# Kernel tuning notes

Measured on AMD Instinct MI355X. Metric: run time of the kernel, lower is better.

The kernel has to match this reference:

```python
import jax, jax.numpy as jnp
import numpy as np

B, H, G, N, D, S, K = 1, 32, 128, 64, 128, 256, 8
BIT_PACK = 8


def setup_inputs() -> dict:
    key = jax.random.key(0)
    ks = jax.random.split(key, 6)
    data = jax.random.normal(ks[0], (B, H, G, N, D), dtype=jnp.float32)
    query = jax.random.normal(ks[1], (B, H, 1, D), dtype=jnp.float32)
    outlier_indices = jax.random.randint(ks[2], (B, H, G, K), 0, D, dtype=jnp.int32)
    norm_data = jax.random.uniform(ks[3], (B, H, G, N), dtype=jnp.float32)
    norm_outlier = jax.random.uniform(ks[4], (B, H, G, N), dtype=jnp.float32)
    # _init_proj_dir + _init_rot_dir (rot=True): per-chunk QR, scaled by sqrt(D)
    proj = np.asarray(jax.random.normal(ks[5], (D, S), dtype=jnp.float32), dtype=np.float64)
    num_chunks = (S + D - 1) // D
    qs = []
    for i in range(num_chunks):
        q, _ = np.linalg.qr(proj[:, i * D:(i + 1) * D])
        qs.append(q)
    proj_dir_score = jnp.asarray(np.concatenate(qs, axis=-1) * np.sqrt(D), dtype=jnp.float32)  # [D, S]
    proj_dir_quant = proj_dir_score.T  # [S, D]
    return {"data": data, "query": query, "outlier_indices": outlier_indices,
            "norm_data": norm_data, "norm_outlier": norm_outlier,
            "proj_dir_quant": proj_dir_quant, "proj_dir_score": proj_dir_score}


def _pack_bits(sketched):
    # sketched: [..., S] -> uint8 packed [..., S//8] ; bit = (sketched > 0)
    x = (sketched > 0).astype(jnp.int32).reshape(*sketched.shape[:-1], -1, BIT_PACK)
    enc = (2 ** jnp.arange(BIT_PACK, dtype=jnp.int32))
    return (x * enc).sum(axis=-1).astype(jnp.uint8)


def reference(data, query, outlier_indices, norm_data, norm_outlier, proj_dir_quant, proj_dir_score):
    s = proj_dir_quant.shape[0]
    d = data.shape[-1]
    # scatter outlier indices into a {0,1} mask over head_dim, per (B,H,G)
    mask = (jax.nn.one_hot(outlier_indices, d, dtype=jnp.float32).sum(axis=-2) > 0).astype(data.dtype)  # [B,H,G,D]
    key_outlier = data * mask[..., None, :]
    key_inlier = data * (1.0 - mask)[..., None, :]
    # JL random projection: [B,H,G,N,D] x [S,D] -> [B,H,G,N,S]
    sk_outlier = jnp.einsum('bhgnd,sd->bhgns', key_outlier, proj_dir_quant)
    sk_inlier = jnp.einsum('bhgnd,sd->bhgns', key_inlier, proj_dir_quant)
    # 1-bit sign quantization + byte packing
    hash_inlier = _pack_bits(sk_inlier)                  # [B,H,G,N,S//8]
    hash_outlier = _pack_bits(sk_outlier)[..., : s // 16]  # truncated outlier sketch
    # score path (PyTorch fallback math): inlier hamming-style inner product
    sketched_q = jnp.einsum('bhqd,ds->bhqs', query, proj_dir_score)[:, :, 0, :]  # [B,H,S]
    bits = jnp.where(sk_inlier > 0, 1.0, -1.0).astype(jnp.float32)  # == unpacked hash_inlier bits *2-1
    ip = jnp.einsum('bhs,bhgns->bhgn', sketched_q, bits)
    scl = jnp.sqrt(jnp.asarray(np.pi / 2, dtype=jnp.float32)) / s
    scores = (scl * norm_data * ip).reshape(data.shape[0], data.shape[1], -1, 1)  # [B,H,G*N,1]
    return hash_inlier, hash_outlier, scores
```

## Files before the change

kernel.cpp:

```cpp
#include <hip/hip_runtime.h>
#include <hip/hip_bf16.h>


typedef __attribute__((ext_vector_type(8))) short short8;
typedef __attribute__((ext_vector_type(4))) float f32x4;

constexpr int cH = 32, cG = 128, cN = 64, cD = 128, cS = 256, cK = 8;
constexpr int HASH_OUT_BASE = cH * cG * cN * (cS / 8);
constexpr int SCORE_BASE    = HASH_OUT_BASE + cH * cG * cN * (cS / 16);
constexpr float EPS_IN  = 1e-3f;
constexpr float EPS_OUT = 1e-3f;
constexpr size_t WS_BHI = 32768, WS_BLO = 98304, WS_NEED = 163840;

#define MFMA(a, b, c) __builtin_amdgcn_mfma_f32_16x16x32_bf16(a, b, c, 0, 0, 0)

__device__ inline short f2bf(float x) {
    unsigned u = __builtin_bit_cast(unsigned, x);
    u += 0x7FFFu + ((u >> 16) & 1u);
    return (short)(u >> 16);
}
__device__ inline float bf2f(short s) {
    return __builtin_bit_cast(float, (unsigned)((unsigned short)s) << 16);
}
__device__ inline unsigned long long sel4(unsigned long long a0, unsigned long long a1,
                                          unsigned long long a2, unsigned long long a3, int r) {
    unsigned long long x = a0;
    x = (r == 1) ? a1 : x; x = (r == 2) ? a2 : x; x = (r == 3) ? a3 : x;
    return x;
}
__device__ inline int sel8(const int* u, int k) {
    int x = u[0];
    x = (k == 1) ? u[1] : x; x = (k == 2) ? u[2] : x; x = (k == 3) ? u[3] : x;
    x = (k == 4) ? u[4] : x; x = (k == 5) ? u[5] : x; x = (k == 6) ? u[6] : x;
    x = (k == 7) ? u[7] : x;
    return x;
}
#define CE(i, j) { int a = u[i], b = u[j]; u[i] = min(a, b); u[j] = max(a, b); }

#define SORT8_AND_MASK(oidx_ptr, bb)                                   \
    int u[cK];                                                         \
    _Pragma("unroll")                                                  \
    for (int k = 0; k < cK; ++k) u[k] = (oidx_ptr)[(bb) * cK + k];     \
    unsigned long long m0 = 0, m1 = 0;                                 \
    _Pragma("unroll")                                                  \
    for (int k = 0; k < cK; ++k) {                                     \
        int v = u[k];                                                  \
        if (v < 64) m0 |= 1ull << v; else m1 |= 1ull << (v - 64);      \
    }                                                                  \
    CE(0,1) CE(2,3) CE(4,5) CE(6,7)                                    \
    CE(0,2) CE(1,3) CE(4,6) CE(5,7)                                    \
    CE(1,2) CE(5,6)                                                    \
    CE(0,4) CE(1,5) CE(2,6) CE(3,7)                                    \
    CE(2,4) CE(3,5)                                                    \
    CE(1,2) CE(3,4) CE(5,6)

__device__ __attribute__((noinline)) float exact_inlier(
    const float* __restrict__ dr, const float* __restrict__ pr,
    unsigned long long m0, unsigned long long m1)
{
    float ex = 0.0f;
    #pragma unroll 1
    for (int dc = 0; dc < 4; ++dc) {
        float4 da[8], pa[8];
        #pragma unroll
        for (int j = 0; j < 8; ++j) {
            da[j] = reinterpret_cast<const float4*>(dr)[dc * 8 + j];
            pa[j] = reinterpret_cast<const float4*>(pr)[dc * 8 + j];
        }
        #pragma unroll
        for (int j = 0; j < 8; ++j) {
            float dv[4] = { da[j].x, da[j].y, da[j].z, da[j].w };
            float pv[4] = { pa[j].x, pa[j].y, pa[j].z, pa[j].w };
            #pragma unroll
            for (int e = 0; e < 4; ++e) {
                const int d = dc * 32 + j * 4 + e;
                const bool msk = ((((d < 64) ? (m0 >> d) : (m1 >> (d - 64))) & 1ull) != 0);
                ex = fmaf(dv[e], msk ? 0.0f : pv[e], ex);
            }
        }
    }
    return ex;
}

__global__ __launch_bounds__(256) void qjl_qv(
    const float* __restrict__ query, const float* __restrict__ projs,
    float* __restrict__ qv_out)
{
    const int h = blockIdx.x, s = threadIdx.x;
    float qa = 0.0f;
    for (int d = 0; d < cD; ++d)
        qa = fmaf(query[h * cD + d], projs[d * cS + s], qa);
    qv_out[h * cS + s] = qa;
}

__global__ __launch_bounds__(256) void qjl_bfrag(
    const float* __restrict__ projq, short* __restrict__ bhi, short* __restrict__ blo)
{
    const int idx = blockIdx.x * 256 + threadIdx.x;
    const int l = idx & 63, nt = (idx >> 6) & 15, ksub = idx >> 10;
    const int s = nt * 16 + (l & 15);
    const int k0 = ksub * 32 + (l >> 4) * 8;
    #pragma unroll
    for (int j = 0; j < 8; ++j) {
        float x = projq[s * cD + k0 + j];
        short h = f2bf(x);
        bhi[idx * 8 + j] = h;
        blo[idx * 8 + j] = f2bf(x - bf2f(h));
    }
}

__global__ __launch_bounds__(256, 3) void qjl_mfma(
    const float* __restrict__ data, const int* __restrict__ oidx,
    const float* __restrict__ norm_data, const float* __restrict__ projq,
    const float* __restrict__ qv_ws, const short* __restrict__ bhi_ws,
    const short* __restrict__ blo_ws, float* __restrict__ out)
{
    const int b    = blockIdx.x;
    const int t    = threadIdx.x;
    const int lane = t & 63;
    const int w    = t >> 6;
    const int c0   = lane & 15;
    const int g16  = lane >> 4;
    const int h    = b >> 7;

    __shared__ short A_hi[16 * 64 * 8];
    __shared__ short A_lo[16 * 64 * 8];
    __shared__ float dO[cK * cN];
    __shared__ float pO[cK * 128];
    __shared__ float ipPart[cN * 4];

    const f32x4 zero4 = { 0.f, 0.f, 0.f, 0.f };

    SORT8_AND_MASK(oidx, b)
    const float* __restrict__ chunk = data + (size_t)b * (cN * cD);

    #pragma unroll
    for (int i = 0; i < 4; ++i) {
        const int slot = i * 256 + t;
        const int l = slot & 63, frag = slot >> 6;
        const int mt = frag & 3, ksub = frag >> 2;
        const int row = mt * 16 + (l & 15);
        const int k0 = ksub * 32 + (l >> 4) * 8;
        const float4* p = reinterpret_cast<const float4*>(chunk + row * cD + k0);
        float4 v0 = p[0], v1 = p[1];
        float xs[8] = { v0.x, v0.y, v0.z, v0.w, v1.x, v1.y, v1.z, v1.w };
        const unsigned bits = (unsigned)(((k0 < 64) ? (m0 >> k0) : (m1 >> (k0 - 64))) & 0xFFull);
        short hs[8], ls[8];
        #pragma unroll
        for (int e = 0; e < 8; ++e) {
            float x = ((bits >> e) & 1u) ? 0.0f : xs[e];
            hs[e] = f2bf(x);
            ls[e] = f2bf(x - bf2f(hs[e]));
        }
        *reinterpret_cast<short8*>(&A_hi[slot * 8]) =
            short8{ hs[0], hs[1], hs[2], hs[3], hs[4], hs[5], hs[6], hs[7] };
        *reinterpret_cast<short8*>(&A_lo[slot * 8]) =
            short8{ ls[0], ls[1], ls[2], ls[3], ls[4], ls[5], ls[6], ls[7] };
    }
    #pragma unroll
    for (int i = 0; i < 2; ++i) {
        const int idx = i * 256 + t;
        const int k = idx >> 6, row = idx & 63;
        dO[idx] = chunk[row * cD + sel8(u, k)];
    }
    #pragma unroll
    for (int i = 0; i < 4; ++i) {
        const int idx = i * 256 + t;
        const int k = idx >> 7, s = idx & 127;
        const int uk = sel8(u, k);
        const bool dup = (k > 0) && (uk == sel8(u, k - 1));
        float x = projq[s * cD + uk];
        pO[idx] = dup ? 0.0f : x;
    }
    __syncthreads();

    if (w < 2) {
        short8 aO[4];
        #pragma unroll
        for (int mt = 0; mt < 4; ++mt) {
            short v8[8];
            #pragma unroll
            for (int k = 0; k < cK; ++k) {
                float x = dO[k * cN + mt * 16 + c0];
                short hi = f2bf(x), lo = f2bf(x - bf2f(hi));
                v8[k] = (g16 == 2) ? lo : ((g16 == 3) ? (short)0 : hi);
            }
            aO[mt] = short8{ v8[0], v8[1], v8[2], v8[3], v8[4], v8[5], v8[6], v8[7] };
        }
        short8 bO[4];
        #pragma unroll
        for (int q = 0; q < 4; ++q) {
            const int s = (w * 4 + q) * 16 + c0;
            short v8[8];
            #pragma unroll
            for (int k = 0; k < cK; ++k) {
                float x = pO[k * 128 + s];
                short hi = f2bf(x), lo = f2bf(x - bf2f(hi));
                v8[k] = (g16 == 1) ? lo : ((g16 == 3) ? (short)0 : hi);
            }
            bO[q] = short8{ v8[0], v8[1], v8[2], v8[3], v8[4], v8[5], v8[6], v8[7] };
        }
        #pragma unroll
        for (int mt = 0; mt < 4; ++mt) {
            #pragma unroll
            for (int q = 0; q < 4; ++q) {
                f32x4 accO = MFMA(aO[mt], bO[q], zero4);
                unsigned long long b0, b1, b2, b3;
                #pragma unroll
                for (int r = 0; r < 4; ++r) {
                    float v = accO[r];
                    if (fabsf(v) < EPS_OUT) {
                        int row = mt * 16 + 4 * g16 + r;
                        int s = (w * 4 + q) * 16 + c0;
                        float o = 0.0f;
                        #pragma unroll
                        for (int k = 0; k < cK; ++k)
                            o = fmaf(dO[k * cN + row], pO[k * 128 + s], o);
                        v = o;
                    }
                    unsigned long long bal = __ballot(v > 0.0f);
                    if (r == 0) b0 = bal; else if (r == 1) b1 = bal;
                    else if (r == 2) b2 = bal; else b3 = bal;
                }
                if (lane < 32) {
                    int r = lane & 3, g = (lane >> 2) & 3, hb = lane >> 4;
                    unsigned long long bb = sel4(b0, b1, b2, b3, r);
                    int row = mt * 16 + 4 * g + r;
                    out[HASH_OUT_BASE + (size_t)b * (cN * 16) + row * 16 + (w * 4 + q) * 2 + hb] =
                        (float)((bb >> (16 * g + 8 * hb)) & 0xFFull);
                }
            }
        }
    }

    f32x4 acc[16];
    #pragma unroll
    for (int i = 0; i < 16; ++i)
        acc[i] = zero4;

    #pragma unroll
    for (int ksub = 0; ksub < 4; ++ksub) {
        short8 ah[4], al[4];
        #pragma unroll
        for (int mt = 0; mt < 4; ++mt) {
            ah[mt] = *reinterpret_cast<const short8*>(&A_hi[((ksub * 4 + mt) * 64 + lane) * 8]);
            al[mt] = *reinterpret_cast<const short8*>(&A_lo[((ksub * 4 + mt) * 64 + lane) * 8]);
        }
        #pragma unroll
        for (int q = 0; q < 4; ++q) {
            short8 bh = *reinterpret_cast<const short8*>(
                &bhi_ws[((ksub * 16 + w * 4 + q) * 64 + lane) * 8]);
            #pragma unroll
            for (int mt = 0; mt < 4; ++mt)
                acc[mt * 4 + q] = MFMA(ah[mt], bh, acc[mt * 4 + q]);
            short8 bl = *reinterpret_cast<const short8*>(
                &blo_ws[((ksub * 16 + w * 4 + q) * 64 + lane) * 8]);
            #pragma unroll
            for (int mt = 0; mt < 4; ++mt)
                acc[mt * 4 + q] = MFMA(ah[mt], bl, acc[mt * 4 + q]);
            #pragma unroll
            for (int mt = 0; mt < 4; ++mt)
                acc[mt * 4 + q] = MFMA(al[mt], bh, acc[mt * 4 + q]);
        }
    }

    float qvv[4];
    #pragma unroll
    for (int q = 0; q < 4; ++q)
        qvv[q] = qv_ws[h * cS + (w * 4 + q) * 16 + c0];

    #pragma unroll
    for (int mt = 0; mt < 4; ++mt) {
        float part[4] = { 0.f, 0.f, 0.f, 0.f };
        #pragma unroll
        for (int q = 0; q < 4; ++q) {
            unsigned long long b0, b1, b2, b3;
            #pragma unroll
            for (int r = 0; r < 4; ++r) {
                float v = acc[mt * 4 + q][r];
                if (fabsf(v) < EPS_IN) {
                    int row = mt * 16 + 4 * g16 + r;
                    int s = (w * 4 + q) * 16 + c0;
                    v = exact_inlier(chunk + row * cD, projq + s * cD, m0, m1);
                }
                bool bit = v > 0.0f;
                unsigned long long bal = __ballot(bit);
                part[r] += bit ? qvv[q] : -qvv[q];
                if (r == 0) b0 = bal; else if (r == 1) b1 = bal;
                else if (r == 2) b2 = bal; else b3 = bal;
            }
            if (lane < 32) {
                int r = lane & 3, g = (lane >> 2) & 3, hb = lane >> 4;
                unsigned long long bb = sel4(b0, b1, b2, b3, r);
                int row = mt * 16 + 4 * g + r;
                out[(size_t)b * (cN * 32) + row * 32 + (w * 4 + q) * 2 + hb] =
                    (float)((bb >> (16 * g + 8 * hb)) & 0xFFull);
            }
        }
        #pragma unroll
        for (int r = 0; r < 4; ++r) {
            float x = part[r];
            x += __shfl_xor(x, 1); x += __shfl_xor(x, 2);
            x += __shfl_xor(x, 4); x += __shfl_xor(x, 8);
            if (c0 == 0) ipPart[(mt * 16 + 4 * g16 + r) * 4 + w] = x;
        }
    }
    __syncthreads();
    if (t < cN) {
        float ip = ipPart[t * 4 + 0] + ipPart[t * 4 + 1]
                 + ipPart[t * 4 + 2] + ipPart[t * 4 + 3];
        const float scl = 0.0048957583f;
        out[SCORE_BASE + (size_t)b * cN + t] = scl * norm_data[b * cN + t] * ip;
    }
}

__global__ __launch_bounds__(256) void qjl_valu(
    const float* __restrict__ data, const float* __restrict__ query,
    const int* __restrict__ oidx, const float* __restrict__ norm_data,
    const float* __restrict__ projq, const float* __restrict__ projs,
    float* __restrict__ out)
{
    const int b2 = blockIdx.x, b = b2 >> 1, half = b2 & 1;
    const int t = threadIdx.x, lane = t & 63, w = t >> 6, h = b >> 7;
    __shared__ float ipPart[32 * 4];
    int u[cK]; int U = 0;
    for (int k = 0; k < cK; ++k) {
        int v = oidx[b * cK + k];
        bool dup = false;
        for (int j = 0; j < U; ++j) dup = dup || (u[j] == v);
        if (!dup) u[U++] = v;
    }
    for (int i = 1; i < U; ++i) {
        int key = u[i], j = i - 1;
        while (j >= 0 && u[j] > key) { u[j + 1] = u[j]; --j; }
        u[j + 1] = key;
    }
    unsigned long long m0 = 0, m1 = 0;
    for (int k = 0; k < U; ++k) {
        int v = u[k];
        if (v < 64) m0 |= 1ull << v; else m1 |= 1ull << (v - 64);
    }
    int ui[cK]; float prO[cK];
    #pragma unroll
    for (int k = 0; k < cK; ++k) ui[k] = (k < U) ? u[k] : 0;
    #pragma unroll
    for (int k = 0; k < cK; ++k) prO[k] = (k < U) ? projq[t * cD + ui[k]] : 0.0f;
    float qv = 0.0f;
    for (int d = 0; d < cD; ++d)
        qv = fmaf(query[h * cD + d], projs[d * cS + t], qv);
    const float* __restrict__ chunk = data + (size_t)b * (cN * cD) + half * (32 * cD);
    float acc[32];
    #pragma unroll
    for (int n = 0; n < 32; ++n) acc[n] = 0.0f;
    for (int dc = 0; dc < cD / 16; ++dc) {
        float pm[16];
        const float4* p4 = reinterpret_cast<const float4*>(projq + t * cD + dc * 16);
        #pragma unroll
        for (int j = 0; j < 4; ++j) {
            float4 v = p4[j];
            float tmp[4] = { v.x, v.y, v.z, v.w };
            #pragma unroll
            for (int e = 0; e < 4; ++e) {
                int d = dc * 16 + j * 4 + e;
                bool msk = (((d < 64) ? (m0 >> d) : (m1 >> (d - 64))) & 1ull) != 0;
                pm[j * 4 + e] = msk ? 0.0f : tmp[e];
            }
        }
        #pragma unroll
        for (int n = 0; n < 32; ++n) {
            const float* __restrict__ r = chunk + n * cD + dc * 16;
            #pragma unroll
            for (int i = 0; i < 16; ++i)
                acc[n] = fmaf(r[i], pm[i], acc[n]);
        }
    }
    #pragma unroll
    for (int n = 0; n < 32; ++n) {
        const int nn = half * 32 + n;
        const float* __restrict__ r = chunk + n * cD;
        float o = 0.0f;
        #pragma unroll
        for (int k = 0; k < cK; ++k)
            o = fmaf((k < U) ? r[ui[k]] : 0.0f, prO[k], o);
        const bool bitIn = acc[n] > 0.0f;
        unsigned long long mIn = __ballot(bitIn);
        unsigned long long mOut = __ballot(o > 0.0f);
        float v = bitIn ? qv : -qv;
        #pragma unroll
        for (int off = 32; off > 0; off >>= 1) v += __shfl_down(v, off);
        if (lane == 0) ipPart[n * 4 + w] = v;
        if (lane < 8) {
            out[(size_t)b * (cN * 32) + nn * 32 + w * 8 + lane] =
                (float)((mIn >> (8 * lane)) & 0xFFull);
            if (w < 2)
                out[HASH_OUT_BASE + (size_t)b * (cN * 16) + nn * 16 + w * 8 + lane] =
                    (float)((mOut >> (8 * lane)) & 0xFFull);
        }
    }
    __syncthreads();
    if (t < 32) {
        float ip = ipPart[t * 4 + 0] + ipPart[t * 4 + 1] + ipPart[t * 4 + 2] + ipPart[t * 4 + 3];
        out[SCORE_BASE + b * cN + half * 32 + t] = 0.0048957583f * norm_data[b * cN + half * 32 + t] * ip;
    }
}

extern "C" void kernel_launch(void* const* d_in, const int* in_sizes, int n_in,
                              void* d_out, int out_size, void* d_ws, size_t ws_size,
                              hipStream_t stream) {
    const float* data      = (const float*)d_in[0];
    const float* query     = (const float*)d_in[1];
    const int*   oidx      = (const int*)d_in[2];
    const float* norm_data = (const float*)d_in[3];
    const float* projq     = (const float*)d_in[5];
    const float* projs     = (const float*)d_in[6];
    float* out = (float*)d_out;

    if (ws_size >= WS_NEED) {
        float* qv  = (float*)d_ws;
        short* bhi = (short*)((char*)d_ws + WS_BHI);
        short* blo = (short*)((char*)d_ws + WS_BLO);
        qjl_qv<<<cH, cS, 0, stream>>>(query, projs, qv);
        qjl_bfrag<<<16, 256, 0, stream>>>(projq, bhi, blo);
        qjl_mfma<<<cH * cG, 256, 0, stream>>>(data, oidx, norm_data, projq,
                                              qv, bhi, blo, out);
    } else {
        qjl_valu<<<cH * cG * 2, 256, 0, stream>>>(data, query, oidx, norm_data,
                                                  projq, projs, out);
    }
}
```

Baseline: 169.1 us.

## Stage hash outputs in shared memory and spread outlier sketch across all waves

Hash bytes for the inlier and outlier sketches are now written into a padded shared-memory buffer that reuses the A_hi/A_lo staging space, then copied to global memory with coalesced float4 stores. Before, each byte was scattered straight to global memory. The outlier MFMA sketch moves after the main inlier GEMM and is split across all four waves (two N-tiles each) instead of two waves doing four. This balances the per-wave work. The cost is an extra barrier and shared-memory reads, and the padded row strides of 33 and 17 are there to avoid bank conflicts.

```diff
diff --git a/kernel.cpp b/kernel.cpp
--- a/kernel.cpp
+++ b/kernel.cpp
@@ -123,11 +123,14 @@
     const int g16  = lane >> 4;
     const int h    = b >> 7;
 
-    __shared__ short A_hi[16 * 64 * 8];
-    __shared__ short A_lo[16 * 64 * 8];
+    __shared__ char  A_buf[32768];
     __shared__ float dO[cK * cN];
     __shared__ float pO[cK * 128];
     __shared__ float ipPart[cN * 4];
+    short* A_hi  = reinterpret_cast<short*>(A_buf);
+    short* A_lo  = reinterpret_cast<short*>(A_buf + 16384);
+    float* hashI = reinterpret_cast<float*>(A_buf);
+    float* hashO = reinterpret_cast<float*>(A_buf + 16384);
 
     const f32x4 zero4 = { 0.f, 0.f, 0.f, 0.f };
 
@@ -174,7 +177,82 @@
     }
     __syncthreads();
 
-    if (w < 2) {
+    f32x4 acc[16];
+    #pragma unroll
+    for (int i = 0; i < 16; ++i)
+        acc[i] = zero4;
+
+    #pragma unroll
+    for (int ksub = 0; ksub < 4; ++ksub) {
+        short8 ah[4], al[4];
+        #pragma unroll
+        for (int mt = 0; mt < 4; ++mt) {
+            ah[mt] = *reinterpret_cast<const short8*>(&A_hi[((ksub * 4 + mt) * 64 + lane) * 8]);
+            al[mt] = *reinterpret_cast<const short8*>(&A_lo[((ksub * 4 + mt) * 64 + lane) * 8]);
+        }
+        #pragma unroll
+        for (int q = 0; q < 4; ++q) {
+            short8 bh = *reinterpret_cast<const short8*>(
+                &bhi_ws[((ksub * 16 + w * 4 + q) * 64 + lane) * 8]);
+            #pragma unroll
+            for (int mt = 0; mt < 4; ++mt)
+                acc[mt * 4 + q] = MFMA(ah[mt], bh, acc[mt * 4 + q]);
+            short8 bl = *reinterpret_cast<const short8*>(
+                &blo_ws[((ksub * 16 + w * 4 + q) * 64 + lane) * 8]);
+            #pragma unroll
+            for (int mt = 0; mt < 4; ++mt)
+                acc[mt * 4 + q] = MFMA(ah[mt], bl, acc[mt * 4 + q]);
+            #pragma unroll
+            for (int mt = 0; mt < 4; ++mt)
+                acc[mt * 4 + q] = MFMA(al[mt], bh, acc[mt * 4 + q]);
+        }
+    }
+
+    __syncthreads();
+
+    float qvv[4];
+    #pragma unroll
+    for (int q = 0; q < 4; ++q)
+        qvv[q] = qv_ws[h * cS + (w * 4 + q) * 16 + c0];
+
+    #pragma unroll
+    for (int mt = 0; mt < 4; ++mt) {
+        float part[4] = { 0.f, 0.f, 0.f, 0.f };
+        #pragma unroll
+        for (int q = 0; q < 4; ++q) {
+            unsigned long long b0, b1, b2, b3;
+            #pragma unroll
+            for (int r = 0; r < 4; ++r) {
+                float v = acc[mt * 4 + q][r];
+                if (fabsf(v) < EPS_IN) {
+                    int row = mt * 16 + 4 * g16 + r;
+                    int s = (w * 4 + q) * 16 + c0;
+                    v = exact_inlier(chunk + row * cD, projq + s * cD, m0, m1);
+                }
+                bool bit = v > 0.0f;
+                unsigned long long bal = __ballot(bit);
+                part[r] += bit ? qvv[q] : -qvv[q];
+                if (r == 0) b0 = bal; else if (r == 1) b1 = bal;
+                else if (r == 2) b2 = bal; else b3 = bal;
+            }
+            if (lane < 32) {
+                int r = lane & 3, g = (lane >> 2) & 3, hb = lane >> 4;
+                unsigned long long bb = sel4(b0, b1, b2, b3, r);
+                int row = mt * 16 + 4 * g + r;
+                hashI[row * 33 + (w * 4 + q) * 2 + hb] =
+                    (float)((bb >> (16 * g + 8 * hb)) & 0xFFull);
+            }
+        }
+        #pragma unroll
+        for (int r = 0; r < 4; ++r) {
+            float x = part[r];
+            x += __shfl_xor(x, 1); x += __shfl_xor(x, 2);
+            x += __shfl_xor(x, 4); x += __shfl_xor(x, 8);
+            if (c0 == 0) ipPart[(mt * 16 + 4 * g16 + r) * 4 + w] = x;
+        }
+    }
+
+    {
         short8 aO[4];
         #pragma unroll
         for (int mt = 0; mt < 4; ++mt) {
@@ -187,10 +265,10 @@
             }
             aO[mt] = short8{ v8[0], v8[1], v8[2], v8[3], v8[4], v8[5], v8[6], v8[7] };
         }
-        short8 bO[4];
-        #pragma unroll
-        for (int q = 0; q < 4; ++q) {
-            const int s = (w * 4 + q) * 16 + c0;
+        #pragma unroll
+        for (int q = 0; q < 2; ++q) {
+            const int ntq = 2 * w + q;
+            const int s = ntq * 16 + c0;
             short v8[8];
             #pragma unroll
             for (int k = 0; k < cK; ++k) {
@@ -198,20 +276,16 @@
                 short hi = f2bf(x), lo = f2bf(x - bf2f(hi));
                 v8[k] = (g16 == 1) ? lo : ((g16 == 3) ? (short)0 : hi);
             }
-            bO[q] = short8{ v8[0], v8[1], v8[2], v8[3], v8[4], v8[5], v8[6], v8[7] };
-        }
-        #pragma unroll
-        for (int mt = 0; mt < 4; ++mt) {
-            #pragma unroll
-            for (int q = 0; q < 4; ++q) {
-                f32x4 accO = MFMA(aO[mt], bO[q], zero4);
+            short8 bO = short8{ v8[0], v8[1], v8[2], v8[3], v8[4], v8[5], v8[6], v8[7] };
+            #pragma unroll
+            for (int mt = 0; mt < 4; ++mt) {
+                f32x4 accO = MFMA(aO[mt], bO, zero4);
                 unsigned long long b0, b1, b2, b3;
                 #pragma unroll
                 for (int r = 0; r < 4; ++r) {
                     float v = accO[r];
                     if (fabsf(v) < EPS_OUT) {
                         int row = mt * 16 + 4 * g16 + r;
-                        int s = (w * 4 + q) * 16 + c0;
                         float o = 0.0f;
                         #pragma unroll
                         for (int k = 0; k < cK; ++k)
@@ -226,86 +300,35 @@
                     int r = lane & 3, g = (lane >> 2) & 3, hb = lane >> 4;
                     unsigned long long bb = sel4(b0, b1, b2, b3, r);
                     int row = mt * 16 + 4 * g + r;
-                    out[HASH_OUT_BASE + (size_t)b * (cN * 16) + row * 16 + (w * 4 + q) * 2 + hb] =
+                    hashO[row * 17 + ntq * 2 + hb] =
                         (float)((bb >> (16 * g + 8 * hb)) & 0xFFull);
                 }
             }
         }
     }
-
-    f32x4 acc[16];
-    #pragma unroll
-    for (int i = 0; i < 16; ++i)
-        acc[i] = zero4;
-
-    #pragma unroll
-    for (int ksub = 0; ksub < 4; ++ksub) {
-        short8 ah[4], al[4];
-        #pragma unroll
-        for (int mt = 0; mt < 4; ++mt) {
-            ah[mt] = *reinterpret_cast<const short8*>(&A_hi[((ksub * 4 + mt) * 64 + lane) * 8]);
-            al[mt] = *reinterpret_cast<const short8*>(&A_lo[((ksub * 4 + mt) * 64 + lane) * 8]);
-        }
-        #pragma unroll
-        for (int q = 0; q < 4; ++q) {
-            short8 bh = *reinterpret_cast<const short8*>(
-                &bhi_ws[((ksub * 16 + w * 4 + q) * 64 + lane) * 8]);
-            #pragma unroll
-            for (int mt = 0; mt < 4; ++mt)
-                acc[mt * 4 + q] = MFMA(ah[mt], bh, acc[mt * 4 + q]);
-            short8 bl = *reinterpret_cast<const short8*>(
-                &blo_ws[((ksub * 16 + w * 4 + q) * 64 + lane) * 8]);
-            #pragma unroll
-            for (int mt = 0; mt < 4; ++mt)
-                acc[mt * 4 + q] = MFMA(ah[mt], bl, acc[mt * 4 + q]);
-            #pragma unroll
-            for (int mt = 0; mt < 4; ++mt)
-                acc[mt * 4 + q] = MFMA(al[mt], bh, acc[mt * 4 + q]);
-        }
-    }
-
-    float qvv[4];
-    #pragma unroll
-    for (int q = 0; q < 4; ++q)
-        qvv[q] = qv_ws[h * cS + (w * 4 + q) * 16 + c0];
-
-    #pragma unroll
-    for (int mt = 0; mt < 4; ++mt) {
-        float part[4] = { 0.f, 0.f, 0.f, 0.f };
-        #pragma unroll
-        for (int q = 0; q < 4; ++q) {
-            unsigned long long b0, b1, b2, b3;
-            #pragma unroll
-            for (int r = 0; r < 4; ++r) {
-                float v = acc[mt * 4 + q][r];
-                if (fabsf(v) < EPS_IN) {
-                    int row = mt * 16 + 4 * g16 + r;
-                    int s = (w * 4 + q) * 16 + c0;
-                    v = exact_inlier(chunk + row * cD, projq + s * cD, m0, m1);
-                }
-                bool bit = v > 0.0f;
-                unsigned long long bal = __ballot(bit);
-                part[r] += bit ? qvv[q] : -qvv[q];
-                if (r == 0) b0 = bal; else if (r == 1) b1 = bal;
-                else if (r == 2) b2 = bal; else b3 = bal;
-            }
-            if (lane < 32) {
-                int r = lane & 3, g = (lane >> 2) & 3, hb = lane >> 4;
-                unsigned long long bb = sel4(b0, b1, b2, b3, r);
-                int row = mt * 16 + 4 * g + r;
-                out[(size_t)b * (cN * 32) + row * 32 + (w * 4 + q) * 2 + hb] =
-                    (float)((bb >> (16 * g + 8 * hb)) & 0xFFull);
-            }
-        }
-        #pragma unroll
-        for (int r = 0; r < 4; ++r) {
-            float x = part[r];
-            x += __shfl_xor(x, 1); x += __shfl_xor(x, 2);
-            x += __shfl_xor(x, 4); x += __shfl_xor(x, 8);
-            if (c0 == 0) ipPart[(mt * 16 + 4 * g16 + r) * 4 + w] = x;
-        }
-    }
     __syncthreads();
+
+    #pragma unroll
+    for (int i = 0; i < 2; ++i) {
+        const int base = t * 8 + i * 4;
+        const int row = base >> 5, col = base & 31;
+        float4 v;
+        v.x = hashI[row * 33 + col + 0];
+        v.y = hashI[row * 33 + col + 1];
+        v.z = hashI[row * 33 + col + 2];
+        v.w = hashI[row * 33 + col + 3];
+        reinterpret_cast<float4*>(out + (size_t)b * (cN * 32))[t * 2 + i] = v;
+    }
+    {
+        const int base = t * 4;
+        const int row = base >> 4, col = base & 15;
+        float4 v;
+        v.x = hashO[row * 17 + col + 0];
+        v.y = hashO[row * 17 + col + 1];
+        v.z = hashO[row * 17 + col + 2];
+        v.w = hashO[row * 17 + col + 3];
+        reinterpret_cast<float4*>(out + HASH_OUT_BASE + (size_t)b * (cN * 16))[t] = v;
+    }
     if (t < cN) {
         float ip = ipPart[t * 4 + 0] + ipPart[t * 4 + 1]
                  + ipPart[t * 4 + 2] + ipPart[t * 4 + 3];
```

Result: no change. 166.9 us (-1.3%).

## Split each MFMA block into two half-row blocks to double grid size

Applied to the files above, without the earlier changes.

Each (h,g) chunk of 64 rows is now handled by two blocks of 32 rows each. The grid doubles and per-block LDS and accumulator registers are halved. This aims to raise occupancy and parallelism across CUs and cut register pressure. The cost is that per-block setup is duplicated: the outlier mask sort, the pO projection gather and the outlier B-fragment conversion, plus reloading the B fragments from workspace.

```diff
diff --git a/kernel.cpp b/kernel.cpp
--- a/kernel.cpp
+++ b/kernel.cpp
@@ -115,19 +115,22 @@
     const float* __restrict__ qv_ws, const short* __restrict__ bhi_ws,
     const short* __restrict__ blo_ws, float* __restrict__ out)
 {
-    const int b    = blockIdx.x;
+    const int b2   = blockIdx.x;
+    const int b    = b2 >> 1;
+    const int half = b2 & 1;
     const int t    = threadIdx.x;
     const int lane = t & 63;
     const int w    = t >> 6;
     const int c0   = lane & 15;
     const int g16  = lane >> 4;
     const int h    = b >> 7;
-
-    __shared__ short A_hi[16 * 64 * 8];
-    __shared__ short A_lo[16 * 64 * 8];
-    __shared__ float dO[cK * cN];
+    const int rowbase = half * 32;
+
+    __shared__ short A_hi[8 * 64 * 8];
+    __shared__ short A_lo[8 * 64 * 8];
+    __shared__ float dO[cK * 32];
     __shared__ float pO[cK * 128];
-    __shared__ float ipPart[cN * 4];
+    __shared__ float ipPart[32 * 4];
 
     const f32x4 zero4 = { 0.f, 0.f, 0.f, 0.f };
 
@@ -135,11 +138,11 @@
     const float* __restrict__ chunk = data + (size_t)b * (cN * cD);
 
     #pragma unroll
-    for (int i = 0; i < 4; ++i) {
+    for (int i = 0; i < 2; ++i) {
         const int slot = i * 256 + t;
         const int l = slot & 63, frag = slot >> 6;
-        const int mt = frag & 3, ksub = frag >> 2;
-        const int row = mt * 16 + (l & 15);
+        const int mt = frag & 1, ksub = frag >> 1;
+        const int row = rowbase + mt * 16 + (l & 15);
         const int k0 = ksub * 32 + (l >> 4) * 8;
         const float4* p = reinterpret_cast<const float4*>(chunk + row * cD + k0);
         float4 v0 = p[0], v1 = p[1];
@@ -157,11 +160,9 @@
         *reinterpret_cast<short8*>(&A_lo[slot * 8]) =
             short8{ ls[0], ls[1], ls[2], ls[3], ls[4], ls[5], ls[6], ls[7] };
     }
-    #pragma unroll
-    for (int i = 0; i < 2; ++i) {
-        const int idx = i * 256 + t;
-        const int k = idx >> 6, row = idx & 63;
-        dO[idx] = chunk[row * cD + sel8(u, k)];
+    {
+        const int k = t >> 5, row = t & 31;
+        dO[t] = chunk[(rowbase + row) * cD + sel8(u, k)];
     }
     #pragma unroll
     for (int i = 0; i < 4; ++i) {
@@ -175,19 +176,18 @@
     __syncthreads();
 
     if (w < 2) {
-        short8 aO[4];
-        #pragma unroll
-        for (int mt = 0; mt < 4; ++mt) {
+        short8 aO[2];
+        #pragma unroll
+        for (int mt = 0; mt < 2; ++mt) {
             short v8[8];
             #pragma unroll
             for (int k = 0; k < cK; ++k) {
-                float x = dO[k * cN + mt * 16 + c0];
+                float x = dO[k * 32 + mt * 16 + c0];
                 short hi = f2bf(x), lo = f2bf(x - bf2f(hi));
                 v8[k] = (g16 == 2) ? lo : ((g16 == 3) ? (short)0 : hi);
             }
             aO[mt] = short8{ v8[0], v8[1], v8[2], v8[3], v8[4], v8[5], v8[6], v8[7] };
         }
-        short8 bO[4];
         #pragma unroll
         for (int q = 0; q < 4; ++q) {
             const int s = (w * 4 + q) * 16 + c0;
@@ -198,24 +198,20 @@
                 short hi = f2bf(x), lo = f2bf(x - bf2f(hi));
                 v8[k] = (g16 == 1) ? lo : ((g16 == 3) ? (short)0 : hi);
             }
-            bO[q] = short8{ v8[0], v8[1], v8[2], v8[3], v8[4], v8[5], v8[6], v8[7] };
-        }
-        #pragma unroll
-        for (int mt = 0; mt < 4; ++mt) {
-            #pragma unroll
-            for (int q = 0; q < 4; ++q) {
-                f32x4 accO = MFMA(aO[mt], bO[q], zero4);
+            short8 bO = short8{ v8[0], v8[1], v8[2], v8[3], v8[4], v8[5], v8[6], v8[7] };
+            #pragma unroll
+            for (int mt = 0; mt < 2; ++mt) {
+                f32x4 accO = MFMA(aO[mt], bO, zero4);
                 unsigned long long b0, b1, b2, b3;
                 #pragma unroll
                 for (int r = 0; r < 4; ++r) {
                     float v = accO[r];
                     if (fabsf(v) < EPS_OUT) {
-                        int row = mt * 16 + 4 * g16 + r;
-                        int s = (w * 4 + q) * 16 + c0;
+                        int rl = mt * 16 + 4 * g16 + r;
                         float o = 0.0f;
                         #pragma unroll
                         for (int k = 0; k < cK; ++k)
-                            o = fmaf(dO[k * cN + row], pO[k * 128 + s], o);
+                            o = fmaf(dO[k * 32 + rl], pO[k * 128 + s], o);
                         v = o;
                     }
                     unsigned long long bal = __ballot(v > 0.0f);
@@ -225,7 +221,7 @@
                 if (lane < 32) {
                     int r = lane & 3, g = (lane >> 2) & 3, hb = lane >> 4;
                     unsigned long long bb = sel4(b0, b1, b2, b3, r);
-                    int row = mt * 16 + 4 * g + r;
+                    int row = rowbase + mt * 16 + 4 * g + r;
                     out[HASH_OUT_BASE + (size_t)b * (cN * 16) + row * 16 + (w * 4 + q) * 2 + hb] =
                         (float)((bb >> (16 * g + 8 * hb)) & 0xFFull);
                 }
@@ -233,33 +229,33 @@
         }
     }
 
-    f32x4 acc[16];
-    #pragma unroll
-    for (int i = 0; i < 16; ++i)
+    f32x4 acc[8];
+    #pragma unroll
+    for (int i = 0; i < 8; ++i)
         acc[i] = zero4;
 
     #pragma unroll
     for (int ksub = 0; ksub < 4; ++ksub) {
-        short8 ah[4], al[4];
-        #pragma unroll
-        for (int mt = 0; mt < 4; ++mt) {
-            ah[mt] = *reinterpret_cast<const short8*>(&A_hi[((ksub * 4 + mt) * 64 + lane) * 8]);
-            al[mt] = *reinterpret_cast<const short8*>(&A_lo[((ksub * 4 + mt) * 64 + lane) * 8]);
+        short8 ah[2], al[2];
+        #pragma unroll
+        for (int mt = 0; mt < 2; ++mt) {
+            ah[mt] = *reinterpret_cast<const short8*>(&A_hi[((ksub * 2 + mt) * 64 + lane) * 8]);
+            al[mt] = *reinterpret_cast<const short8*>(&A_lo[((ksub * 2 + mt) * 64 + lane) * 8]);
         }
         #pragma unroll
         for (int q = 0; q < 4; ++q) {
             short8 bh = *reinterpret_cast<const short8*>(
                 &bhi_ws[((ksub * 16 + w * 4 + q) * 64 + lane) * 8]);
             #pragma unroll
-            for (int mt = 0; mt < 4; ++mt)
+            for (int mt = 0; mt < 2; ++mt)
                 acc[mt * 4 + q] = MFMA(ah[mt], bh, acc[mt * 4 + q]);
             short8 bl = *reinterpret_cast<const short8*>(
                 &blo_ws[((ksub * 16 + w * 4 + q) * 64 + lane) * 8]);
             #pragma unroll
-            for (int mt = 0; mt < 4; ++mt)
+            for (int mt = 0; mt < 2; ++mt)
                 acc[mt * 4 + q] = MFMA(ah[mt], bl, acc[mt * 4 + q]);
             #pragma unroll
-            for (int mt = 0; mt < 4; ++mt)
+            for (int mt = 0; mt < 2; ++mt)
                 acc[mt * 4 + q] = MFMA(al[mt], bh, acc[mt * 4 + q]);
         }
     }
@@ -270,7 +266,7 @@
         qvv[q] = qv_ws[h * cS + (w * 4 + q) * 16 + c0];
 
     #pragma unroll
-    for (int mt = 0; mt < 4; ++mt) {
+    for (int mt = 0; mt < 2; ++mt) {
         float part[4] = { 0.f, 0.f, 0.f, 0.f };
         #pragma unroll
         for (int q = 0; q < 4; ++q) {
@@ -279,7 +275,7 @@
             for (int r = 0; r < 4; ++r) {
                 float v = acc[mt * 4 + q][r];
                 if (fabsf(v) < EPS_IN) {
-                    int row = mt * 16 + 4 * g16 + r;
+                    int row = rowbase + mt * 16 + 4 * g16 + r;
                     int s = (w * 4 + q) * 16 + c0;
                     v = exact_inlier(chunk + row * cD, projq + s * cD, m0, m1);
                 }
@@ -292,7 +288,7 @@
             if (lane < 32) {
                 int r = lane & 3, g = (lane >> 2) & 3, hb = lane >> 4;
                 unsigned long long bb = sel4(b0, b1, b2, b3, r);
-                int row = mt * 16 + 4 * g + r;
+                int row = rowbase + mt * 16 + 4 * g + r;
                 out[(size_t)b * (cN * 32) + row * 32 + (w * 4 + q) * 2 + hb] =
                     (float)((bb >> (16 * g + 8 * hb)) & 0xFFull);
             }
@@ -306,11 +302,12 @@
         }
     }
     __syncthreads();
-    if (t < cN) {
+    if (t < 32) {
         float ip = ipPart[t * 4 + 0] + ipPart[t * 4 + 1]
                  + ipPart[t * 4 + 2] + ipPart[t * 4 + 3];
         const float scl = 0.0048957583f;
-        out[SCORE_BASE + (size_t)b * cN + t] = scl * norm_data[b * cN + t] * ip;
+        out[SCORE_BASE + (size_t)b * cN + rowbase + t] =
+            scl * norm_data[b * cN + rowbase + t] * ip;
     }
 }
 
@@ -421,8 +418,8 @@
         short* blo = (short*)((char*)d_ws + WS_BLO);
         qjl_qv<<<cH, cS, 0, stream>>>(query, projs, qv);
         qjl_bfrag<<<16, 256, 0, stream>>>(projq, bhi, blo);
-        qjl_mfma<<<cH * cG, 256, 0, stream>>>(data, oidx, norm_data, projq,
-                                              qv, bhi, blo, out);
+        qjl_mfma<<<cH * cG * 2, 256, 0, stream>>>(data, oidx, norm_data, projq,
+                                                  qv, bhi, blo, out);
     } else {
         qjl_valu<<<cH * cG * 2, 256, 0, stream>>>(data, query, oidx, norm_data,
                                                   projq, projs, out);
```

Measured after the change: 193.6 us. +14.5%, slower.
